# Kernel tuning notes

Measured on AMD Instinct MI355X. Metric: run time of the kernel, lower is better.

The kernel has to match this reference:

```python
import jax, jax.numpy as jnp
import numpy as np

N = 400000      # active voxels
INC = 64
OUTC = 64
GRID = 128      # voxel grid extent per axis
K = 27          # 3x3x3 kernel offsets
EPS = 1e-5      # BatchNorm eps


def setup_inputs() -> dict:
    rng = np.random.default_rng(0)
    # unique sorted voxel keys in a GRID^3 volume (hash = linearized coord)
    flat = np.sort(rng.choice(GRID ** 3, size=N, replace=False)).astype(np.int64)
    cx = flat // (GRID * GRID)
    cy = (flat // GRID) % GRID
    cz = flat % GRID
    offsets = [(dx, dy, dz) for dx in (-1, 0, 1) for dy in (-1, 0, 1) for dz in (-1, 0, 1)]
    in_idx = np.zeros((K, N), np.int32)
    out_idx = np.zeros((K, N), np.int32)
    mask = np.zeros((K, N), np.float32)
    # kernel map: for each offset, hash-lookup which input voxels have an output voxel at coord+offset
    for k, (dx, dy, dz) in enumerate(offsets):
        nx, ny, nz = cx + dx, cy + dy, cz + dz
        valid = (nx >= 0) & (nx < GRID) & (ny >= 0) & (ny < GRID) & (nz >= 0) & (nz < GRID)
        nkey = nx * GRID * GRID + ny * GRID + nz
        pos = np.searchsorted(flat, nkey)
        pos_c = np.clip(pos, 0, N - 1)
        found = valid & (flat[pos_c] == nkey)
        src = np.nonzero(found)[0]
        dst = pos_c[src]
        p = src.size
        in_idx[k, :p] = src
        out_idx[k, :p] = dst
        mask[k, :p] = 1.0
    key = jax.random.key(0)
    k1, k2 = jax.random.split(key, 2)
    feats = jax.random.normal(k1, (N, INC), jnp.float32)
    W = jax.random.normal(k2, (K, INC, OUTC), jnp.float32) * (1.0 / np.sqrt(INC * K))
    gamma = jnp.ones((OUTC,), jnp.float32)
    beta = jnp.zeros((OUTC,), jnp.float32)
    return {
        "feats": feats,
        "W": W,
        "gamma": gamma,
        "beta": beta,
        "pair_mask": jnp.asarray(mask),
        "in_idx": jnp.asarray(in_idx),
        "out_idx": jnp.asarray(out_idx),
    }


def reference(feats, W, gamma, beta, pair_mask, in_idx, out_idx):
    # sparse transposed conv3d as gather -> matmul -> scatter-add per kernel offset
    n, outc = feats.shape[0], W.shape[2]
    out = jnp.zeros((n, outc), feats.dtype)
    for k in range(W.shape[0]):  # fixed small loop over 27 kernel offsets
        g = feats[in_idx[k]] * pair_mask[k][:, None]   # [N, INC], padded pairs zeroed
        out = out.at[out_idx[k]].add(g @ W[k])         # scatter into output voxels
    # BatchNorm (training-mode batch stats over voxels) + ReLU
    mean = out.mean(axis=0)
    var = out.var(axis=0)
    y = (out - mean) * jax.lax.rsqrt(var + EPS) * gamma + beta
    return jax.nn.relu(y)
```

## Files before the change

### kernel.cpp

```cpp
#include <hip/hip_runtime.h>
#include <stdint.h>

typedef unsigned short u16;
typedef unsigned int u32;

#define NV 400000
#define KOFF 27
#define EPS_BN 1e-5f

#define INV_ELEMS (KOFF * NV)
#define INV_BYTES (INV_ELEMS * 4)
#define FEATSBF_OFF INV_BYTES
#define WT_OFF (FEATSBF_OFF + NV * 64 * 2)
#define STATS_OFF (WT_OFF + KOFF * 64 * 64 * 2)

using short8 = __attribute__((ext_vector_type(8))) short;
using floatx16 = __attribute__((ext_vector_type(16))) float;

__device__ __forceinline__ u16 f2bf(float f) {
  u32 u = __float_as_uint(f);
  u += 0x7FFFu + ((u >> 16) & 1u);
  return (u16)(u >> 16);
}

__global__ void k_init(int* __restrict__ inv, float* __restrict__ stats) {
  int i = blockIdx.x * 256 + threadIdx.x;
  if (i < INV_ELEMS / 4) ((int4*)inv)[i] = make_int4(-1, -1, -1, -1);
  if (blockIdx.x == 0) stats[threadIdx.x] = 0.0f;
}

__global__ void k_cvt(const float* __restrict__ feats, u16* __restrict__ featsBf) {
  int i = blockIdx.x * 256 + threadIdx.x;
  if (i >= NV * 64 / 4) return;
  float4 v = ((const float4*)feats)[i];
  ushort4 o;
  o.x = f2bf(v.x); o.y = f2bf(v.y); o.z = f2bf(v.z); o.w = f2bf(v.w);
  ((ushort4*)featsBf)[i] = o;
}

__global__ void k_build(const int* __restrict__ in_idx, const int* __restrict__ out_idx,
                        const float* __restrict__ mask, int* __restrict__ inv) {
  int t = blockIdx.x * 256 + threadIdx.x;
  if (t >= INV_ELEMS) return;
  if (mask[t] != 0.0f) {
    int k = t / NV;
    inv[k * NV + out_idx[t]] = in_idx[t];
  }
}

__global__ void k_wt(const float* __restrict__ W, u16* __restrict__ Wt) {
  int t = blockIdx.x * 256 + threadIdx.x;
  if (t >= KOFF * 64 * 64) return;
  int k = t >> 12, rem = t & 4095, c = rem >> 6, o = rem & 63;
  Wt[(k << 12) + (o << 6) + c] = f2bf(W[t]);
}

__global__ void __launch_bounds__(256)
k_main(const u16* __restrict__ feats, const int* __restrict__ inv,
       const u16* __restrict__ Wt, float* __restrict__ out, float* __restrict__ stats) {
  __shared__ u16 Wsm[2][64][72];
  __shared__ float redS[4][64];
  __shared__ float redQ[4][64];

  const int t = threadIdx.x;
  const int lane = t & 63;
  const int wave = t >> 6;
  const int lo = lane & 31;
  const int hi = lane >> 5;
  const int rbase = blockIdx.x * 256 + wave * 64;
  const int row0 = rbase + lo;
  const int row1 = rbase + 32 + lo;

  const floatx16 z16 = {0.f, 0.f, 0.f, 0.f, 0.f, 0.f, 0.f, 0.f,
                        0.f, 0.f, 0.f, 0.f, 0.f, 0.f, 0.f, 0.f};
  floatx16 acc00 = z16, acc01 = z16, acc10 = z16, acc11 = z16;

  const int wr0 = t >> 3;
  const int wc0 = (t & 7) * 8;

  uint4 w0 = *(const uint4*)(Wt + t * 8);
  uint4 w1 = *(const uint4*)(Wt + (t + 256) * 8);
  int psrc0 = (row0 < NV) ? inv[row0] : -1;
  int psrc1 = (row1 < NV) ? inv[row1] : -1;

  for (int k = 0; k < KOFF; ++k) {
    const int buf = k & 1;
    *(uint4*)&Wsm[buf][wr0][wc0] = w0;
    *(uint4*)&Wsm[buf][wr0 + 32][wc0] = w1;
    const int src0 = psrc0, src1 = psrc1;
    if (k + 1 < KOFF) {
      const u16* wk = Wt + ((k + 1) << 12);
      w0 = *(const uint4*)(wk + t * 8);
      w1 = *(const uint4*)(wk + (t + 256) * 8);
      const int* ik = inv + (k + 1) * NV;
      psrc0 = (row0 < NV) ? ik[row0] : -1;
      psrc1 = (row1 < NV) ? ik[row1] : -1;
    }
    const short8 z8 = {0, 0, 0, 0, 0, 0, 0, 0};
    short8 A0[4], A1[4];
#pragma unroll
    for (int kk = 0; kk < 4; ++kk) { A0[kk] = z8; A1[kk] = z8; }
    if (src0 >= 0) {
      const u16* p = feats + src0 * 64 + hi * 8;
      A0[0] = *(const short8*)(p);
      A0[1] = *(const short8*)(p + 16);
      A0[2] = *(const short8*)(p + 32);
      A0[3] = *(const short8*)(p + 48);
    }
    if (src1 >= 0) {
      const u16* p = feats + src1 * 64 + hi * 8;
      A1[0] = *(const short8*)(p);
      A1[1] = *(const short8*)(p + 16);
      A1[2] = *(const short8*)(p + 32);
      A1[3] = *(const short8*)(p + 48);
    }
    __syncthreads();
#pragma unroll
    for (int kk = 0; kk < 4; ++kk) {
      short8 b0 = *(const short8*)&Wsm[buf][lo][kk * 16 + hi * 8];
      short8 b1 = *(const short8*)&Wsm[buf][32 + lo][kk * 16 + hi * 8];
      acc00 = __builtin_amdgcn_mfma_f32_32x32x16_bf16(A0[kk], b0, acc00, 0, 0, 0);
      acc01 = __builtin_amdgcn_mfma_f32_32x32x16_bf16(A0[kk], b1, acc01, 0, 0, 0);
      acc10 = __builtin_amdgcn_mfma_f32_32x32x16_bf16(A1[kk], b0, acc10, 0, 0, 0);
      acc11 = __builtin_amdgcn_mfma_f32_32x32x16_bf16(A1[kk], b1, acc11, 0, 0, 0);
    }
  }

  float s0 = 0.f, q0 = 0.f, s1 = 0.f, q1 = 0.f;
#pragma unroll
  for (int r = 0; r < 16; ++r) {
    s0 += acc00[r] + acc10[r];
    q0 += acc00[r] * acc00[r] + acc10[r] * acc10[r];
    s1 += acc01[r] + acc11[r];
    q1 += acc01[r] * acc01[r] + acc11[r] * acc11[r];
  }
  s0 += __shfl_xor(s0, 32, 64); q0 += __shfl_xor(q0, 32, 64);
  s1 += __shfl_xor(s1, 32, 64); q1 += __shfl_xor(q1, 32, 64);
  if (lane < 32) {
    redS[wave][lo] = s0; redQ[wave][lo] = q0;
    redS[wave][32 + lo] = s1; redQ[wave][32 + lo] = q1;
  }

#pragma unroll
  for (int r = 0; r < 16; ++r) {
    int rl = (r & 3) + ((r >> 2) * 8) + hi * 4;
    int ra = rbase + rl;
    int rb = rbase + 32 + rl;
    if (ra < NV) { out[ra * 64 + lo] = acc00[r]; out[ra * 64 + 32 + lo] = acc01[r]; }
    if (rb < NV) { out[rb * 64 + lo] = acc10[r]; out[rb * 64 + 32 + lo] = acc11[r]; }
  }

  __syncthreads();
  if (t < 64) {
    float s = redS[0][t] + redS[1][t] + redS[2][t] + redS[3][t];
    float q = redQ[0][t] + redQ[1][t] + redQ[2][t] + redQ[3][t];
    atomicAdd(&stats[t], s);
    atomicAdd(&stats[64 + t], q);
  }
}

__global__ void k_stats(const float* __restrict__ stats, const float* __restrict__ gamma,
                        const float* __restrict__ beta, float* __restrict__ sc,
                        float* __restrict__ sh) {
  int t = threadIdx.x;
  float inv_n = 1.0f / (float)NV;
  float mean = stats[t] * inv_n;
  float var = stats[64 + t] * inv_n - mean * mean;
  float scale = gamma[t] * rsqrtf(var + EPS_BN);
  sc[t] = scale;
  sh[t] = beta[t] - mean * scale;
}

__global__ void k_apply(float* __restrict__ out, const float* __restrict__ sc,
                        const float* __restrict__ sh) {
  int i = blockIdx.x * 256 + threadIdx.x;
  if (i >= NV * 64 / 4) return;
  int c0 = (i & 15) * 4;
  float4 v = ((const float4*)out)[i];
  float* pv = (float*)&v;
#pragma unroll
  for (int j = 0; j < 4; ++j) {
    float y = pv[j] * sc[c0 + j] + sh[c0 + j];
    pv[j] = y > 0.f ? y : 0.f;
  }
  ((float4*)out)[i] = v;
}

extern "C" void kernel_launch(void* const* d_in, const int* in_sizes, int n_in,
                              void* d_out, int out_size, void* d_ws, size_t ws_size,
                              hipStream_t stream) {
  const float* feats = (const float*)d_in[0];
  const float* W     = (const float*)d_in[1];
  const float* gamma = (const float*)d_in[2];
  const float* beta  = (const float*)d_in[3];
  const float* mask  = (const float*)d_in[4];
  const int* in_idx  = (const int*)d_in[5];
  const int* out_idx = (const int*)d_in[6];
  float* out = (float*)d_out;

  char* ws = (char*)d_ws;
  int* inv = (int*)ws;
  u16* featsBf = (u16*)(ws + FEATSBF_OFF);
  u16* Wt = (u16*)(ws + WT_OFF);
  float* stats = (float*)(ws + STATS_OFF);

  k_init<<<(INV_ELEMS / 4 + 255) / 256, 256, 0, stream>>>(inv, stats);
  k_cvt<<<(NV * 64 / 4 + 255) / 256, 256, 0, stream>>>(feats, featsBf);
  k_build<<<(INV_ELEMS + 255) / 256, 256, 0, stream>>>(in_idx, out_idx, mask, inv);
  k_wt<<<(KOFF * 4096 + 255) / 256, 256, 0, stream>>>(W, Wt);
  k_main<<<(NV + 255) / 256, 256, 0, stream>>>(featsBf, inv, Wt, out, stats);
  k_stats<<<1, 64, 0, stream>>>(stats, gamma, beta, stats + 128, stats + 192);
  k_apply<<<(NV * 64 / 4 + 255) / 256, 256, 0, stream>>>(out, stats + 128, stats + 192);
}
```

Before: 423.1 us.

## Merge prep kernels, prefetch next gather in main loop, fold stats into apply

The three preprocessing kernels (feature bf16 conversion, inverse-map build, weight transpose) become one launch that dispatches on block index, and the inverse-map init becomes a hipMemsetAsync. The main MFMA loop is unrolled by two with ping-pong register buffers, so the feature gather for offset k+1 is issued before the MFMAs for offset k, and index loads run two offsets ahead. The one-block stats kernel is folded into the apply kernel, where each block recomputes scale and shift into shared memory. This removes launch overhead and hides gather latency, at the cost of more registers in the main kernel and a possible drop in occupancy.

```diff
diff --git a/kernel.cpp b/kernel.cpp
--- a/kernel.cpp
+++ b/kernel.cpp
@@ -14,6 +14,11 @@
 #define WT_OFF (FEATSBF_OFF + NV * 64 * 2)
 #define STATS_OFF (WT_OFF + KOFF * 64 * 64 * 2)
 
+#define CVT_BLOCKS 25000
+#define BUILD_BLOCKS 42188
+#define WT_BLOCKS 432
+#define PREP_BLOCKS (CVT_BLOCKS + BUILD_BLOCKS + WT_BLOCKS)
+
 using short8 = __attribute__((ext_vector_type(8))) short;
 using floatx16 = __attribute__((ext_vector_type(16))) float;
 
@@ -23,36 +28,31 @@
   return (u16)(u >> 16);
 }
 
-__global__ void k_init(int* __restrict__ inv, float* __restrict__ stats) {
-  int i = blockIdx.x * 256 + threadIdx.x;
-  if (i < INV_ELEMS / 4) ((int4*)inv)[i] = make_int4(-1, -1, -1, -1);
-  if (blockIdx.x == 0) stats[threadIdx.x] = 0.0f;
-}
-
-__global__ void k_cvt(const float* __restrict__ feats, u16* __restrict__ featsBf) {
-  int i = blockIdx.x * 256 + threadIdx.x;
-  if (i >= NV * 64 / 4) return;
-  float4 v = ((const float4*)feats)[i];
-  ushort4 o;
-  o.x = f2bf(v.x); o.y = f2bf(v.y); o.z = f2bf(v.z); o.w = f2bf(v.w);
-  ((ushort4*)featsBf)[i] = o;
-}
-
-__global__ void k_build(const int* __restrict__ in_idx, const int* __restrict__ out_idx,
-                        const float* __restrict__ mask, int* __restrict__ inv) {
-  int t = blockIdx.x * 256 + threadIdx.x;
-  if (t >= INV_ELEMS) return;
-  if (mask[t] != 0.0f) {
-    int k = t / NV;
-    inv[k * NV + out_idx[t]] = in_idx[t];
-  }
-}
-
-__global__ void k_wt(const float* __restrict__ W, u16* __restrict__ Wt) {
-  int t = blockIdx.x * 256 + threadIdx.x;
-  if (t >= KOFF * 64 * 64) return;
-  int k = t >> 12, rem = t & 4095, c = rem >> 6, o = rem & 63;
-  Wt[(k << 12) + (o << 6) + c] = f2bf(W[t]);
+__global__ void k_prep(const float* __restrict__ feats, u16* __restrict__ featsBf,
+                       const int* __restrict__ in_idx, const int* __restrict__ out_idx,
+                       const float* __restrict__ mask, int* __restrict__ inv,
+                       const float* __restrict__ W, u16* __restrict__ Wt) {
+  const int b = blockIdx.x;
+  const int tid = threadIdx.x;
+  if (b < CVT_BLOCKS) {
+    int i = b * 256 + tid;
+    float4 v = ((const float4*)feats)[i];
+    ushort4 o;
+    o.x = f2bf(v.x); o.y = f2bf(v.y); o.z = f2bf(v.z); o.w = f2bf(v.w);
+    ((ushort4*)featsBf)[i] = o;
+  } else if (b < CVT_BLOCKS + BUILD_BLOCKS) {
+    int t = (b - CVT_BLOCKS) * 256 + tid;
+    if (t < INV_ELEMS && mask[t] != 0.0f) {
+      int k = t / NV;
+      inv[k * NV + out_idx[t]] = in_idx[t];
+    }
+  } else {
+    int t = (b - CVT_BLOCKS - BUILD_BLOCKS) * 256 + tid;
+    if (t < KOFF * 64 * 64) {
+      int k = t >> 12, rem = t & 4095, c = rem >> 6, o = rem & 63;
+      Wt[(k << 12) + (o << 6) + c] = f2bf(W[t]);
+    }
+  }
 }
 
 __global__ void __launch_bounds__(256)
@@ -70,6 +70,8 @@
   const int rbase = blockIdx.x * 256 + wave * 64;
   const int row0 = rbase + lo;
   const int row1 = rbase + 32 + lo;
+  const bool v0 = row0 < NV;
+  const bool v1 = row1 < NV;
 
   const floatx16 z16 = {0.f, 0.f, 0.f, 0.f, 0.f, 0.f, 0.f, 0.f,
                         0.f, 0.f, 0.f, 0.f, 0.f, 0.f, 0.f, 0.f};
@@ -78,53 +80,85 @@
   const int wr0 = t >> 3;
   const int wc0 = (t & 7) * 8;
 
-  uint4 w0 = *(const uint4*)(Wt + t * 8);
-  uint4 w1 = *(const uint4*)(Wt + (t + 256) * 8);
-  int psrc0 = (row0 < NV) ? inv[row0] : -1;
-  int psrc1 = (row1 < NV) ? inv[row1] : -1;
-
-  for (int k = 0; k < KOFF; ++k) {
-    const int buf = k & 1;
-    *(uint4*)&Wsm[buf][wr0][wc0] = w0;
-    *(uint4*)&Wsm[buf][wr0 + 32][wc0] = w1;
-    const int src0 = psrc0, src1 = psrc1;
+#define GATHER(A0, A1, s0, s1)                                        \
+  {                                                                   \
+    const short8 z8 = {0, 0, 0, 0, 0, 0, 0, 0};                       \
+    A0[0] = z8; A0[1] = z8; A0[2] = z8; A0[3] = z8;                   \
+    A1[0] = z8; A1[1] = z8; A1[2] = z8; A1[3] = z8;                   \
+    if ((s0) >= 0) {                                                  \
+      const u16* p = feats + (s0) * 64 + hi * 8;                      \
+      A0[0] = *(const short8*)(p);                                    \
+      A0[1] = *(const short8*)(p + 16);                               \
+      A0[2] = *(const short8*)(p + 32);                               \
+      A0[3] = *(const short8*)(p + 48);                               \
+    }                                                                 \
+    if ((s1) >= 0) {                                                  \
+      const u16* p = feats + (s1) * 64 + hi * 8;                      \
+      A1[0] = *(const short8*)(p);                                    \
+      A1[1] = *(const short8*)(p + 16);                               \
+      A1[2] = *(const short8*)(p + 32);                               \
+      A1[3] = *(const short8*)(p + 48);                               \
+    }                                                                 \
+  }
+
+#define DOMFMA(BUF, A0, A1)                                                     \
+  _Pragma("unroll")                                                             \
+  for (int kk = 0; kk < 4; ++kk) {                                              \
+    short8 b0 = *(const short8*)&Wsm[BUF][lo][kk * 16 + hi * 8];                \
+    short8 b1 = *(const short8*)&Wsm[BUF][32 + lo][kk * 16 + hi * 8];           \
+    acc00 = __builtin_amdgcn_mfma_f32_32x32x16_bf16(A0[kk], b0, acc00, 0, 0, 0);\
+    acc01 = __builtin_amdgcn_mfma_f32_32x32x16_bf16(A0[kk], b1, acc01, 0, 0, 0);\
+    acc10 = __builtin_amdgcn_mfma_f32_32x32x16_bf16(A1[kk], b0, acc10, 0, 0, 0);\
+    acc11 = __builtin_amdgcn_mfma_f32_32x32x16_bf16(A1[kk], b1, acc11, 0, 0, 0);\
+  }
+
+  uint4 wEa = *(const uint4*)(Wt + t * 8);
+  uint4 wEb = *(const uint4*)(Wt + (t + 256) * 8);
+  uint4 wOa = wEa, wOb = wEb;
+  int sC0 = v0 ? inv[row0] : -1;
+  int sC1 = v1 ? inv[row1] : -1;
+  int sO0 = v0 ? inv[NV + row0] : -1;
+  int sO1 = v1 ? inv[NV + row1] : -1;
+  int sE0 = -1, sE1 = -1;
+
+  short8 Ac0[4], Ac1[4], An0[4], An1[4];
+  GATHER(Ac0, Ac1, sC0, sC1);
+
+  for (int k = 0; k < KOFF; k += 2) {
+    *(uint4*)&Wsm[0][wr0][wc0] = wEa;
+    *(uint4*)&Wsm[0][wr0 + 32][wc0] = wEb;
     if (k + 1 < KOFF) {
       const u16* wk = Wt + ((k + 1) << 12);
-      w0 = *(const uint4*)(wk + t * 8);
-      w1 = *(const uint4*)(wk + (t + 256) * 8);
-      const int* ik = inv + (k + 1) * NV;
-      psrc0 = (row0 < NV) ? ik[row0] : -1;
-      psrc1 = (row1 < NV) ? ik[row1] : -1;
-    }
-    const short8 z8 = {0, 0, 0, 0, 0, 0, 0, 0};
-    short8 A0[4], A1[4];
-#pragma unroll
-    for (int kk = 0; kk < 4; ++kk) { A0[kk] = z8; A1[kk] = z8; }
-    if (src0 >= 0) {
-      const u16* p = feats + src0 * 64 + hi * 8;
-      A0[0] = *(const short8*)(p);
-      A0[1] = *(const short8*)(p + 16);
-      A0[2] = *(const short8*)(p + 32);
-      A0[3] = *(const short8*)(p + 48);
-    }
-    if (src1 >= 0) {
-      const u16* p = feats + src1 * 64 + hi * 8;
-      A1[0] = *(const short8*)(p);
-      A1[1] = *(const short8*)(p + 16);
-      A1[2] = *(const short8*)(p + 32);
-      A1[3] = *(const short8*)(p + 48);
-    }
+      wOa = *(const uint4*)(wk + t * 8);
+      wOb = *(const uint4*)(wk + (t + 256) * 8);
+    }
+    if (k + 2 < KOFF) {
+      const int* ik = inv + (k + 2) * NV;
+      sE0 = v0 ? ik[row0] : -1;
+      sE1 = v1 ? ik[row1] : -1;
+    }
+    if (k + 1 < KOFF) GATHER(An0, An1, sO0, sO1);
     __syncthreads();
-#pragma unroll
-    for (int kk = 0; kk < 4; ++kk) {
-      short8 b0 = *(const short8*)&Wsm[buf][lo][kk * 16 + hi * 8];
-      short8 b1 = *(const short8*)&Wsm[buf][32 + lo][kk * 16 + hi * 8];
-      acc00 = __builtin_amdgcn_mfma_f32_32x32x16_bf16(A0[kk], b0, acc00, 0, 0, 0);
-      acc01 = __builtin_amdgcn_mfma_f32_32x32x16_bf16(A0[kk], b1, acc01, 0, 0, 0);
-      acc10 = __builtin_amdgcn_mfma_f32_32x32x16_bf16(A1[kk], b0, acc10, 0, 0, 0);
-      acc11 = __builtin_amdgcn_mfma_f32_32x32x16_bf16(A1[kk], b1, acc11, 0, 0, 0);
-    }
-  }
+    DOMFMA(0, Ac0, Ac1);
+    if (k + 1 >= KOFF) break;
+    *(uint4*)&Wsm[1][wr0][wc0] = wOa;
+    *(uint4*)&Wsm[1][wr0 + 32][wc0] = wOb;
+    if (k + 2 < KOFF) {
+      const u16* wk = Wt + ((k + 2) << 12);
+      wEa = *(const uint4*)(wk + t * 8);
+      wEb = *(const uint4*)(wk + (t + 256) * 8);
+    }
+    if (k + 3 < KOFF) {
+      const int* ik = inv + (k + 3) * NV;
+      sO0 = v0 ? ik[row0] : -1;
+      sO1 = v1 ? ik[row1] : -1;
+    }
+    if (k + 2 < KOFF) GATHER(Ac0, Ac1, sE0, sE1);
+    __syncthreads();
+    DOMFMA(1, An0, An1);
+  }
+#undef GATHER
+#undef DOMFMA
 
   float s0 = 0.f, q0 = 0.f, s1 = 0.f, q1 = 0.f;
 #pragma unroll
@@ -159,21 +193,20 @@
   }
 }
 
-__global__ void k_stats(const float* __restrict__ stats, const float* __restrict__ gamma,
-                        const float* __restrict__ beta, float* __restrict__ sc,
-                        float* __restrict__ sh) {
-  int t = threadIdx.x;
-  float inv_n = 1.0f / (float)NV;
-  float mean = stats[t] * inv_n;
-  float var = stats[64 + t] * inv_n - mean * mean;
-  float scale = gamma[t] * rsqrtf(var + EPS_BN);
-  sc[t] = scale;
-  sh[t] = beta[t] - mean * scale;
-}
-
-__global__ void k_apply(float* __restrict__ out, const float* __restrict__ sc,
-                        const float* __restrict__ sh) {
-  int i = blockIdx.x * 256 + threadIdx.x;
+__global__ void k_apply(float* __restrict__ out, const float* __restrict__ stats,
+                        const float* __restrict__ gamma, const float* __restrict__ beta) {
+  __shared__ float sc[64], sh[64];
+  const int t = threadIdx.x;
+  if (t < 64) {
+    float inv_n = 1.0f / (float)NV;
+    float mean = stats[t] * inv_n;
+    float var = stats[64 + t] * inv_n - mean * mean;
+    float scale = gamma[t] * rsqrtf(var + EPS_BN);
+    sc[t] = scale;
+    sh[t] = beta[t] - mean * scale;
+  }
+  __syncthreads();
+  int i = blockIdx.x * 256 + t;
   if (i >= NV * 64 / 4) return;
   int c0 = (i & 15) * 4;
   float4 v = ((const float4*)out)[i];
@@ -204,11 +237,9 @@
   u16* Wt = (u16*)(ws + WT_OFF);
   float* stats = (float*)(ws + STATS_OFF);
 
-  k_init<<<(INV_ELEMS / 4 + 255) / 256, 256, 0, stream>>>(inv, stats);
-  k_cvt<<<(NV * 64 / 4 + 255) / 256, 256, 0, stream>>>(feats, featsBf);
-  k_build<<<(INV_ELEMS + 255) / 256, 256, 0, stream>>>(in_idx, out_idx, mask, inv);
-  k_wt<<<(KOFF * 4096 + 255) / 256, 256, 0, stream>>>(W, Wt);
+  hipMemsetAsync(inv, 0xFF, INV_BYTES, stream);
+  hipMemsetAsync(stats, 0, 128 * sizeof(float), stream);
+  k_prep<<<PREP_BLOCKS, 256, 0, stream>>>(feats, featsBf, in_idx, out_idx, mask, inv, W, Wt);
   k_main<<<(NV + 255) / 256, 256, 0, stream>>>(featsBf, inv, Wt, out, stats);
-  k_stats<<<1, 64, 0, stream>>>(stats, gamma, beta, stats + 128, stats + 192);
-  k_apply<<<(NV * 64 / 4 + 255) / 256, 256, 0, stream>>>(out, stats + 128, stats + 192);
-}
+  k_apply<<<NV * 64 / 4 / 256, 256, 0, stream>>>(out, stats, gamma, beta);
+}
```

Result: faster. 404.4 us (-4.4%).
